# Performance work log

Measured on AMD Instinct MI355X. Metric: run time of the kernel, lower is better.

Reference implementation:

```python
import jax, jax.numpy as jnp
import numpy as np

B, L, DIM = 4, 4096, 1024
H, DQK, DV, DINNER, CHUNK = 16, 64, 64, 64, 64
BASE_LR, BASE_WD = 1e-3, 0.9


def setup_inputs() -> dict:
    key = jax.random.key(0)
    ks = jax.random.split(key, 9)
    def s(k, shape, scale):
        return jax.random.normal(k, shape, jnp.float32) * scale
    return {
        "x": jax.random.normal(ks[0], (B, L, DIM), jnp.float32),
        "Wq": s(ks[1], (H * DQK, DIM), DIM ** -0.5),
        "Wk": s(ks[2], (H * DQK, DIM), DIM ** -0.5),
        "Wv": s(ks[3], (H * DV, DIM), DIM ** -0.5),
        "Wlr": s(ks[4], (2 * H, DIM), DIM ** -0.5),
        "Wbeta": s(ks[5], (2 * H, DIM), DIM ** -0.5),
        "Wo": s(ks[6], (DIM, H * DV), (H * DV) ** -0.5),
        "W_in_init": s(ks[7], (1, DINNER, H, DQK), DQK ** -0.5),
        "W_out_init": s(ks[8], (1, DINNER, H, DV), DINNER ** -0.5),
    }


def reference(x, Wq, Wk, Wv, Wlr, Wbeta, Wo, W_in_init, W_out_init):
    b, l, _ = x.shape
    nc = l // CHUNK
    # projections + silu feature map on q/k (feature_map='silu')
    q = jax.nn.silu(x @ Wq.T).reshape(b, l, H, DQK)
    k = jax.nn.silu(x @ Wk.T).reshape(b, l, H, DQK)
    v = (x @ Wv.T).reshape(b, l, H, DV)
    # per-token, per-head gates: lr for (W_in, W_out) and weight-decay gates
    lr = jax.nn.sigmoid(x @ Wlr.T) * BASE_LR     # [b, l, 2H]
    wd = jax.nn.sigmoid(x @ Wbeta.T) * BASE_WD   # [b, l, 2H]

    def chunked(t):  # [b, l, ...] -> [nc, b, CHUNK, ...]
        return jnp.moveaxis(t.reshape(b, nc, CHUNK, *t.shape[2:]), 1, 0)

    qc, kc, vc = chunked(q), chunked(k), chunked(v)
    lr_c = chunked(lr).mean(axis=2)  # [nc, b, 2H], chunk-mean gate
    wd_c = chunked(wd).mean(axis=2)
    lr_in, lr_out = lr_c[..., :H], lr_c[..., H:]
    wd_in, wd_out = wd_c[..., :H], wd_c[..., H:]

    W_in0 = jnp.broadcast_to(W_in_init, (b, DINNER, H, DQK))
    W_out0 = jnp.broadcast_to(W_out_init, (b, DINNER, H, DV))

    def step(carry, xs):
        W_in, W_out = carry
        qi, ki, vi, li, lo, wi, wo = xs
        # readout with current fast weights (softmax over chunk dim n)
        p_q = jax.nn.softmax(jnp.einsum('bnhd,bDhd->bnhD', qi, W_in), axis=1)
        o = jnp.einsum('bnhD,bDhd->bnhd', p_q, W_out)
        # mlp_backprop(k, v, W_in, W_out): fast-weight gradients
        p = jax.nn.softmax(jnp.einsum('bnhd,bDhd->bnhD', ki, W_in), axis=1)
        grad_out = jnp.einsum('bnhD,bnhd->bDhd', -p, vi)
        a = jnp.einsum('bDhd,bnhd->bnhD', W_out, vi)
        s = jnp.sum(p * a, axis=-1, keepdims=True)
        g_z = -(p * a - p * s)
        grad_in = jnp.einsum('bnhd,bnhD->bDhd', ki, g_z)
        # decayed SGD update with data-dependent per-head gates
        W_in = wi[:, None, :, None] * W_in - li[:, None, :, None] * grad_in
        W_out = wo[:, None, :, None] * W_out - lo[:, None, :, None] * grad_out
        return (W_in, W_out), o

    _, outs = jax.lax.scan(step, (W_in0, W_out0),
                           (qc, kc, vc, lr_in, lr_out, wd_in, wd_out))
    # [nc, b, CHUNK, H, DV] -> [b, l, H*DV]
    o = jnp.moveaxis(outs, 0, 1).reshape(b, l, H * DV)
    return o @ Wo.T
```

## Files before the change

### kernel.cpp

```cpp
#include <hip/hip_runtime.h>
#include <stdint.h>

typedef unsigned short u16;
typedef uint32_t u32;
typedef __attribute__((ext_vector_type(4))) float f32x4;
typedef __attribute__((ext_vector_type(8))) short bf16x8;

#define DEVINL __device__ __forceinline__

DEVINL u16 f2bf(float f) {
    union { float f; u32 u; } a; a.f = f;
    u32 u = a.u;
    return (u16)((u + 0x7fffu + ((u >> 16) & 1u)) >> 16);
}
DEVINL u32 pk2(float a, float b) { return (u32)f2bf(a) | ((u32)f2bf(b) << 16); }

DEVINL u32 swz128(u32 row, u32 colb) { return row * 128u + (colb ^ ((row & 7u) << 4)); }

DEVINL void gload_lds16(const u16* g, char* l) {
    __builtin_amdgcn_global_load_lds(
        (const __attribute__((address_space(1))) void*)g,
        (__attribute__((address_space(3))) void*)l, 16, 0, 0);
}

DEVINL float frcp(float x) { float r; asm("v_rcp_f32 %0, %1" : "=v"(r) : "v"(x)); return r; }

template<int C> DEVINL float fdpp(float x) {
    union { float f; int i; } a, b; a.f = x;
    b.i = __builtin_amdgcn_update_dpp(0, a.i, C, 0xf, 0xf, false);
    return b.f;
}
DEVINL float rmax16(float v) {
    v = fmaxf(v, fdpp<0x128>(v)); v = fmaxf(v, fdpp<0x124>(v));
    v = fmaxf(v, fdpp<0x122>(v)); v = fmaxf(v, fdpp<0x121>(v)); return v;
}
DEVINL float rsum16(float v) {
    v += fdpp<0x128>(v); v += fdpp<0x124>(v);
    v += fdpp<0x122>(v); v += fdpp<0x121>(v); return v;
}

DEVINL f32x4 trans4(f32x4 v, int q) {
    float s0 = fdpp<0xB1>(v[0]), s1 = fdpp<0xB1>(v[1]),
          s2 = fdpp<0xB1>(v[2]), s3 = fdpp<0xB1>(v[3]);
    f32x4 t;
    bool q1 = (q & 1) != 0;
    t[0] = q1 ? s1 : v[0];
    t[1] = q1 ? v[1] : s0;
    t[2] = q1 ? s3 : v[2];
    t[3] = q1 ? v[3] : s2;
    float u0 = fdpp<0x4E>(t[0]), u1 = fdpp<0x4E>(t[1]),
          u2 = fdpp<0x4E>(t[2]), u3 = fdpp<0x4E>(t[3]);
    f32x4 r;
    bool q2 = (q & 2) != 0;
    r[0] = q2 ? u2 : t[0];
    r[1] = q2 ? u3 : t[1];
    r[2] = q2 ? t[2] : u0;
    r[3] = q2 ? t[3] : u1;
    return r;
}

__global__ __launch_bounds__(256) void convert_kernel(
    const float* __restrict__ x, const float* __restrict__ Wq,
    const float* __restrict__ Wk, const float* __restrict__ Wv,
    const float* __restrict__ Wo, const float* __restrict__ Wlr,
    const float* __restrict__ Wbeta,
    u16* __restrict__ xb, u16* __restrict__ wb, u16* __restrict__ wob,
    u16* __restrict__ wlb)
{
    const int t0 = blockIdx.x * 256 + threadIdx.x;
    const int stride = gridDim.x * 256;
    auto cv = [&](const float* src, u16* dst, int n4) {
        for (int i = t0; i < n4; i += stride) {
            float4 v = ((const float4*)src)[i];
            uint2 p;
            p.x = pk2(v.x, v.y);
            p.y = pk2(v.z, v.w);
            ((uint2*)dst)[i] = p;
        }
    };
    cv(x, xb, 4194304);
    cv(Wq, wb, 262144);
    cv(Wk, wb + 1048576, 262144);
    cv(Wv, wb + 2097152, 262144);
    cv(Wo, wob, 262144);
    cv(Wlr, wlb, 8192);
    cv(Wbeta, wlb + 32768, 8192);
}

__global__ __launch_bounds__(256) void proj_qkv_kernel(
    const u16* __restrict__ xb, const u16* __restrict__ wb,
    u16* __restrict__ qb, u16* __restrict__ kb, u16* __restrict__ vb)
{
    __shared__ __align__(16) char As[128 * 128];
    __shared__ __align__(16) char Bs[128 * 128];
    const int bn = blockIdx.x;
    const int bm = blockIdx.y;
    const int wsel = bn >> 3;
    u16* __restrict__ dst = (wsel == 0) ? qb : ((wsel == 1) ? kb : vb);
    const int cb = (bn & 7) * 128;
    const int wrow = bn * 128;
    const int rb = bm * 128;
    const int tid = threadIdx.x;
    const int lane = tid & 63;
    const int wv = tid >> 6;
    const int wr = (wv >> 1) * 64, wc = (wv & 1) * 64;
    const int li = lane & 15, g = lane >> 4;
    const int lr8 = lane >> 3, lc8 = lane & 7;

    f32x4 acc[4][4];
#pragma unroll
    for (int i = 0; i < 4; ++i)
#pragma unroll
        for (int j = 0; j < 4; ++j) acc[i][j] = (f32x4)0.0f;

    for (int k0 = 0; k0 < 1024; k0 += 64) {
        __syncthreads();
#pragma unroll
        for (int ld = 0; ld < 4; ++ld) {
            int r0 = wv * 32 + ld * 8;
            int rowT = r0 + lr8;
            int csw = (lc8 * 8) ^ ((rowT & 7) << 3);
            gload_lds16(xb + (size_t)(rb + rowT) * 1024 + k0 + csw, As + r0 * 128);
            gload_lds16(wb + (size_t)(wrow + rowT) * 1024 + k0 + csw, Bs + r0 * 128);
        }
        __syncthreads();
#pragma unroll
        for (int ks = 0; ks < 2; ++ks) {
            bf16x8 af[4], bfr[4];
#pragma unroll
            for (int m = 0; m < 4; ++m)
                af[m] = *(const bf16x8*)(As + swz128(wr + m * 16 + li, ks * 64 + g * 16));
#pragma unroll
            for (int n = 0; n < 4; ++n)
                bfr[n] = *(const bf16x8*)(Bs + swz128(wc + n * 16 + li, ks * 64 + g * 16));
#pragma unroll
            for (int m = 0; m < 4; ++m)
#pragma unroll
                for (int n = 0; n < 4; ++n)
                    acc[m][n] = __builtin_amdgcn_mfma_f32_16x16x32_bf16(af[m], bfr[n], acc[m][n], 0, 0, 0);
        }
    }
    const bool do_silu = (wsel < 2);
#pragma unroll
    for (int m = 0; m < 4; ++m) {
        int t = rb + wr + m * 16 + g * 4;
#pragma unroll
        for (int r = 0; r < 4; ++r) {
#pragma unroll
            for (int n = 0; n < 4; ++n) {
                float v = acc[m][n][r];
                if (do_silu) v = v / (1.0f + __expf(-v));
                int col = cb + wc + n * 16 + li;
                dst[(size_t)(t + r) * 1024 + col] = f2bf(v);
            }
        }
    }
}

__global__ __launch_bounds__(256) void lrwd_kernel(
    const u16* __restrict__ xb, const u16* __restrict__ wlb,
    float* __restrict__ lrc_all)
{
    __shared__ __align__(16) char As[128 * 128];
    __shared__ __align__(16) char Bs[64 * 128];
    __shared__ float red[128][65];
    const int bm = blockIdx.x;
    const int rb = bm * 128;
    const int tid = threadIdx.x;
    const int lane = tid & 63;
    const int wv = tid >> 6;
    const int li = lane & 15, g = lane >> 4;
    const int lr8 = lane >> 3, lc8 = lane & 7;

    f32x4 acc[2][4];
#pragma unroll
    for (int i = 0; i < 2; ++i)
#pragma unroll
        for (int j = 0; j < 4; ++j) acc[i][j] = (f32x4)0.0f;

    for (int k0 = 0; k0 < 1024; k0 += 64) {
        __syncthreads();
#pragma unroll
        for (int ld = 0; ld < 4; ++ld) {
            int r0 = wv * 32 + ld * 8;
            int rowT = r0 + lr8;
            int csw = (lc8 * 8) ^ ((rowT & 7) << 3);
            gload_lds16(xb + (size_t)(rb + rowT) * 1024 + k0 + csw, As + r0 * 128);
        }
#pragma unroll
        for (int ld = 0; ld < 2; ++ld) {
            int r0 = wv * 16 + ld * 8;
            int rowT = r0 + lr8;
            int csw = (lc8 * 8) ^ ((rowT & 7) << 3);
            gload_lds16(wlb + (size_t)rowT * 1024 + k0 + csw, Bs + r0 * 128);
        }
        __syncthreads();
#pragma unroll
        for (int ks = 0; ks < 2; ++ks) {
            bf16x8 af[2], bfr[4];
#pragma unroll
            for (int m = 0; m < 2; ++m)
                af[m] = *(const bf16x8*)(As + swz128(wv * 32 + m * 16 + li, ks * 64 + g * 16));
#pragma unroll
            for (int n = 0; n < 4; ++n)
                bfr[n] = *(const bf16x8*)(Bs + swz128(n * 16 + li, ks * 64 + g * 16));
#pragma unroll
            for (int m = 0; m < 2; ++m)
#pragma unroll
                for (int n = 0; n < 4; ++n)
                    acc[m][n] = __builtin_amdgcn_mfma_f32_16x16x32_bf16(af[m], bfr[n], acc[m][n], 0, 0, 0);
        }
    }
#pragma unroll
    for (int m = 0; m < 2; ++m) {
#pragma unroll
        for (int n = 0; n < 4; ++n) {
            int col = n * 16 + li;
            float scale = (col < 32) ? 1e-3f : 0.9f;
#pragma unroll
            for (int r = 0; r < 4; ++r) {
                int t = wv * 32 + m * 16 + g * 4 + r;
                float s = acc[m][n][r];
                red[t][col] = scale / (1.0f + __expf(-s));
            }
        }
    }
    __syncthreads();
    if (tid < 128) {
        int chunk = tid >> 6, col = tid & 63;
        float s = 0.f;
#pragma unroll
        for (int i = 0; i < 64; ++i) s += red[chunk * 64 + i][col];
        int b = bm >> 5;
        int cidx = (bm & 31) * 2 + chunk;
        lrc_all[((size_t)(b * 64 + cidx)) * 64 + col] = s * (1.0f / 64.0f);
    }
}

__global__ __launch_bounds__(512) void scan_kernel(
    const u16* __restrict__ qb, const u16* __restrict__ kb, const u16* __restrict__ vb,
    const float* __restrict__ lrc_all, const float* __restrict__ Wi0,
    const float* __restrict__ Wo0, u16* __restrict__ ob)
{
    const int bh = blockIdx.x;
    const int b = bh >> 4, h = bh & 15;
    const int tid = threadIdx.x;
    const int lane = tid & 63;
    const int w8 = tid >> 6;
    const bool isA = (w8 < 4);
    const int wq = w8;
    const int wk = w8 - 4;
    const int li = lane & 15, g = lane >> 4;
    const int q4 = li & 3, b4 = li & 12;

    __shared__ __align__(16) char SQ2[2][8192];
    __shared__ __align__(16) char Kc2[2][8192];
    __shared__ __align__(16) char Vc2[2][8192];
    __shared__ __align__(16) char KcT2[2][8192];
    __shared__ __align__(16) char VcT2[2][8192];
    __shared__ __align__(16) char SWoT2[2][8192];
    __shared__ __align__(16) char SWiN[8192];
    __shared__ __align__(16) char SWoN[8192];
    __shared__ __align__(16) char SPQ[8192];
    __shared__ __align__(16) char SPTN[8192];
    __shared__ __align__(16) char SGZN[8192];
    __shared__ float spart[256];
    __shared__ float lrc[256];
    __shared__ u32 cntA, cntB;

    if (tid == 0) { cntA = 0u; cntB = 0u; }

    f32x4 WiR[4], WoR[4];
    if (!isA) {
#pragma unroll
        for (int tn = 0; tn < 4; ++tn) {
            int d = tn * 16 + li;
#pragma unroll
            for (int r = 0; r < 4; ++r) {
                int D = wk * 16 + g * 4 + r;
                WiR[tn][r] = Wi0[((size_t)D * 16 + h) * 64 + d];
                WoR[tn][r] = Wo0[((size_t)D * 16 + h) * 64 + d];
            }
            *(uint2*)(SWoT2[0] + swz128(d, wk * 32 + g * 8)) =
                make_uint2(pk2(WoR[tn][0], WoR[tn][1]), pk2(WoR[tn][2], WoR[tn][3]));
            f32x4 ti = trans4(WiR[tn], q4);
            *(uint2*)(SWiN + swz128(wk * 16 + g * 4 + q4, tn * 32 + b4 * 2)) =
                make_uint2(pk2(ti[0], ti[1]), pk2(ti[2], ti[3]));
            f32x4 to = trans4(WoR[tn], q4);
            *(uint2*)(SWoN + swz128(wk * 16 + g * 4 + q4, tn * 32 + b4 * 2)) =
                make_uint2(pk2(to[0], to[1]), pk2(to[2], to[3]));
        }
    }
    if (tid < 256) {
        int cc = tid >> 2, j = tid & 3;
        lrc[cc * 4 + j] = lrc_all[((size_t)(b * 64 + cc)) * 64 + j * 16 + h];
    }

    const int nb4 = ((tid & 255) >> 4) * 4;
    const int db4 = (tid & 15) * 4;
    uint4 pq_[2];
    uint2 pk_[4], pv_[4];
    auto prefetch = [&](int c) {
        const size_t base = ((size_t)(b * 4096 + c * 64)) * 1024 + h * 64;
#pragma unroll
        for (int p = 0; p < 2; ++p) {
            int id = p * 256 + (tid & 255);
            int n = id >> 3;
            int d0 = (id & 7) * 8;
            pq_[p] = *(const uint4*)(qb + base + (size_t)n * 1024 + d0);
        }
#pragma unroll
        for (int j = 0; j < 4; ++j) {
            pk_[j] = *(const uint2*)(kb + base + (size_t)(nb4 + j) * 1024 + db4);
            pv_[j] = *(const uint2*)(vb + base + (size_t)(nb4 + j) * 1024 + db4);
        }
    };
    auto commit = [&](int buf) {
#pragma unroll
        for (int p = 0; p < 2; ++p) {
            int id = p * 256 + (tid & 255);
            int n = id >> 3;
            int d0 = (id & 7) * 8;
            *(uint4*)(SQ2[buf] + swz128(n, d0 * 2)) = pq_[p];
        }
#pragma unroll
        for (int j = 0; j < 4; ++j) {
            *(uint2*)(Kc2[buf] + swz128(nb4 + j, db4 * 2)) = pk_[j];
            *(uint2*)(Vc2[buf] + swz128(nb4 + j, db4 * 2)) = pv_[j];
        }
#pragma unroll
        for (int i = 0; i < 4; ++i) {
            u32 k0 = (((i & 2) ? pk_[0].y : pk_[0].x) >> ((i & 1) * 16)) & 0xffffu;
            u32 k1 = (((i & 2) ? pk_[1].y : pk_[1].x) >> ((i & 1) * 16)) & 0xffffu;
            u32 k2 = (((i & 2) ? pk_[2].y : pk_[2].x) >> ((i & 1) * 16)) & 0xffffu;
            u32 k3 = (((i & 2) ? pk_[3].y : pk_[3].x) >> ((i & 1) * 16)) & 0xffffu;
            *(uint2*)(KcT2[buf] + swz128(db4 + i, nb4 * 2)) =
                make_uint2(k0 | (k1 << 16), k2 | (k3 << 16));
            u32 v0 = (((i & 2) ? pv_[0].y : pv_[0].x) >> ((i & 1) * 16)) & 0xffffu;
            u32 v1 = (((i & 2) ? pv_[1].y : pv_[1].x) >> ((i & 1) * 16)) & 0xffffu;
            u32 v2 = (((i & 2) ? pv_[2].y : pv_[2].x) >> ((i & 1) * 16)) & 0xffffu;
            u32 v3 = (((i & 2) ? pv_[3].y : pv_[3].x) >> ((i & 1) * 16)) & 0xffffu;
            *(uint2*)(VcT2[buf] + swz128(db4 + i, nb4 * 2)) =
                make_uint2(v0 | (v1 << 16), v2 | (v3 << 16));
        }
    };

    if (isA) { prefetch(0); commit(0); }
    __syncthreads();

    for (int c = 0; c < 64; ++c) {
        const int cur = c & 1, nxt = cur ^ 1;
        f32x4 pk[4], aT[4], go[4];

        if (isA) {
            if (c + 1 < 64) prefetch(c + 1);
            bf16x8 wiA0 = *(const bf16x8*)(SWiN + swz128(wq * 16 + li, g * 16));
            bf16x8 wiA1 = *(const bf16x8*)(SWiN + swz128(wq * 16 + li, 64 + g * 16));
            f32x4 sq[4];
            __builtin_amdgcn_s_setprio(1);
#pragma unroll
            for (int tn = 0; tn < 4; ++tn) {
                bf16x8 b0 = *(const bf16x8*)(SQ2[cur] + swz128(tn * 16 + li, g * 16));
                bf16x8 b1 = *(const bf16x8*)(SQ2[cur] + swz128(tn * 16 + li, 64 + g * 16));
                f32x4 z = (f32x4)0.0f;
                z = __builtin_amdgcn_mfma_f32_16x16x32_bf16(wiA0, b0, z, 0, 0, 0);
                z = __builtin_amdgcn_mfma_f32_16x16x32_bf16(wiA1, b1, z, 0, 0, 0);
                sq[tn] = z;
            }
            __builtin_amdgcn_s_setprio(0);
#pragma unroll
            for (int r = 0; r < 4; ++r) {
                float m = fmaxf(fmaxf(sq[0][r], sq[1][r]), fmaxf(sq[2][r], sq[3][r]));
                m = rmax16(m);
                float e0 = __expf(sq[0][r] - m), e1 = __expf(sq[1][r] - m);
                float e2 = __expf(sq[2][r] - m), e3 = __expf(sq[3][r] - m);
                float inv = frcp(rsum16(e0 + e1 + e2 + e3));
                sq[0][r] = e0 * inv; sq[1][r] = e1 * inv; sq[2][r] = e2 * inv; sq[3][r] = e3 * inv;
            }
#pragma unroll
            for (int tn = 0; tn < 4; ++tn) {
                int n = tn * 16 + li;
                *(uint2*)(SPQ + swz128(n, (wq * 16 + g * 4) * 2)) =
                    make_uint2(pk2(sq[tn][0], sq[tn][1]), pk2(sq[tn][2], sq[tn][3]));
            }
            if (c + 1 < 64) commit(nxt);
            bf16x8 wob0[4], wob1[4];
#pragma unroll
            for (int tn = 0; tn < 4; ++tn) {
                wob0[tn] = *(const bf16x8*)(SWoT2[cur] + swz128(tn * 16 + li, g * 16));
                wob1[tn] = *(const bf16x8*)(SWoT2[cur] + swz128(tn * 16 + li, 64 + g * 16));
            }
            __threadfence_block();
            if (lane == 0) atomicAdd(&cntA, 1u);
            {
                volatile u32* vc = &cntA;
                u32 tgt = 4u * (u32)(c + 1);
                while (*vc < tgt) { __builtin_amdgcn_s_sleep(1); }
            }
            __threadfence_block();
            bf16x8 a0 = *(const bf16x8*)(SPQ + swz128(wq * 16 + li, g * 16));
            bf16x8 a1 = *(const bf16x8*)(SPQ + swz128(wq * 16 + li, 64 + g * 16));
            f32x4 o4[4];
            __builtin_amdgcn_s_setprio(1);
#pragma unroll
            for (int tn = 0; tn < 4; ++tn) {
                f32x4 z = (f32x4)0.0f;
                z = __builtin_amdgcn_mfma_f32_16x16x32_bf16(a0, wob0[tn], z, 0, 0, 0);
                z = __builtin_amdgcn_mfma_f32_16x16x32_bf16(a1, wob1[tn], z, 0, 0, 0);
                o4[tn] = z;
            }
            __builtin_amdgcn_s_setprio(0);
            const size_t obase = ((size_t)(b * 4096 + c * 64)) * 1024 + h * 64;
            const int n_ = wq * 16 + g * 4 + q4;
#pragma unroll
            for (int tn = 0; tn < 4; ++tn) {
                f32x4 to = trans4(o4[tn], q4);
                *(uint2*)(ob + obase + (size_t)n_ * 1024 + tn * 16 + b4) =
                    make_uint2(pk2(to[0], to[1]), pk2(to[2], to[3]));
            }
        } else {
            bf16x8 wiA0 = *(const bf16x8*)(SWiN + swz128(wk * 16 + li, g * 16));
            bf16x8 wiA1 = *(const bf16x8*)(SWiN + swz128(wk * 16 + li, 64 + g * 16));
            __builtin_amdgcn_s_setprio(1);
#pragma unroll
            for (int tn = 0; tn < 4; ++tn) {
                bf16x8 b0 = *(const bf16x8*)(Kc2[cur] + swz128(tn * 16 + li, g * 16));
                bf16x8 b1 = *(const bf16x8*)(Kc2[cur] + swz128(tn * 16 + li, 64 + g * 16));
                f32x4 z = (f32x4)0.0f;
                z = __builtin_amdgcn_mfma_f32_16x16x32_bf16(wiA0, b0, z, 0, 0, 0);
                z = __builtin_amdgcn_mfma_f32_16x16x32_bf16(wiA1, b1, z, 0, 0, 0);
                pk[tn] = z;
            }
            __builtin_amdgcn_s_setprio(0);
#pragma unroll
            for (int r = 0; r < 4; ++r) {
                float m = fmaxf(fmaxf(pk[0][r], pk[1][r]), fmaxf(pk[2][r], pk[3][r]));
                m = rmax16(m);
                float e0 = __expf(pk[0][r] - m), e1 = __expf(pk[1][r] - m);
                float e2 = __expf(pk[2][r] - m), e3 = __expf(pk[3][r] - m);
                float inv = frcp(rsum16(e0 + e1 + e2 + e3));
                pk[0][r] = e0 * inv; pk[1][r] = e1 * inv; pk[2][r] = e2 * inv; pk[3][r] = e3 * inv;
            }
            bf16x8 woA0 = *(const bf16x8*)(SWoN + swz128(wk * 16 + li, g * 16));
            bf16x8 woA1 = *(const bf16x8*)(SWoN + swz128(wk * 16 + li, 64 + g * 16));
            __builtin_amdgcn_s_setprio(1);
#pragma unroll
            for (int tn = 0; tn < 4; ++tn) {
                bf16x8 b0 = *(const bf16x8*)(Vc2[cur] + swz128(tn * 16 + li, g * 16));
                bf16x8 b1 = *(const bf16x8*)(Vc2[cur] + swz128(tn * 16 + li, 64 + g * 16));
                f32x4 z = (f32x4)0.0f;
                z = __builtin_amdgcn_mfma_f32_16x16x32_bf16(woA0, b0, z, 0, 0, 0);
                z = __builtin_amdgcn_mfma_f32_16x16x32_bf16(woA1, b1, z, 0, 0, 0);
                aT[tn] = z;
            }
            __builtin_amdgcn_s_setprio(0);
#pragma unroll
            for (int tn = 0; tn < 4; ++tn) {
                f32x4 t4 = pk[tn] * aT[tn];
                float s_ = t4[0] + t4[1] + t4[2] + t4[3];
                s_ += __shfl_xor(s_, 16);
                s_ += __shfl_xor(s_, 32);
                if (g == 0) spart[wk * 64 + tn * 16 + li] = s_;
            }
#pragma unroll
            for (int tn = 0; tn < 4; ++tn) {
                f32x4 tp = trans4(pk[tn], q4);
                *(uint2*)(SPTN + swz128(wk * 16 + g * 4 + q4, tn * 32 + b4 * 2)) =
                    make_uint2(pk2(tp[0], tp[1]), pk2(tp[2], tp[3]));
            }
            {
                bf16x8 a0 = *(const bf16x8*)(SPTN + swz128(wk * 16 + li, g * 16));
                bf16x8 a1 = *(const bf16x8*)(SPTN + swz128(wk * 16 + li, 64 + g * 16));
                __builtin_amdgcn_s_setprio(1);
#pragma unroll
                for (int tn = 0; tn < 4; ++tn) {
                    bf16x8 b0 = *(const bf16x8*)(VcT2[cur] + swz128(tn * 16 + li, g * 16));
                    bf16x8 b1 = *(const bf16x8*)(VcT2[cur] + swz128(tn * 16 + li, 64 + g * 16));
                    f32x4 z = (f32x4)0.0f;
                    z = __builtin_amdgcn_mfma_f32_16x16x32_bf16(a0, b0, z, 0, 0, 0);
                    z = __builtin_amdgcn_mfma_f32_16x16x32_bf16(a1, b1, z, 0, 0, 0);
                    go[tn] = z;
                }
                __builtin_amdgcn_s_setprio(0);
            }
            bf16x8 kb0[4], kb1[4];
#pragma unroll
            for (int tn = 0; tn < 4; ++tn) {
                kb0[tn] = *(const bf16x8*)(KcT2[cur] + swz128(tn * 16 + li, g * 16));
                kb1[tn] = *(const bf16x8*)(KcT2[cur] + swz128(tn * 16 + li, 64 + g * 16));
            }
            __threadfence_block();
            if (lane == 0) atomicAdd(&cntB, 1u);
            {
                volatile u32* vc = &cntB;
                u32 tgt = 4u * (u32)(c + 1);
                while (*vc < tgt) { __builtin_amdgcn_s_sleep(1); }
            }
            __threadfence_block();
            f32x4 gz[4];
#pragma unroll
            for (int tn = 0; tn < 4; ++tn) {
                int n = tn * 16 + li;
                float sn = spart[n] + spart[64 + n] + spart[128 + n] + spart[192 + n];
#pragma unroll
                for (int r = 0; r < 4; ++r) gz[tn][r] = pk[tn][r] * (sn - aT[tn][r]);
                f32x4 tg = trans4(gz[tn], q4);
                *(uint2*)(SGZN + swz128(wk * 16 + g * 4 + q4, tn * 32 + b4 * 2)) =
                    make_uint2(pk2(tg[0], tg[1]), pk2(tg[2], tg[3]));
            }
            f32x4 gi[4];
            {
                bf16x8 a0 = *(const bf16x8*)(SGZN + swz128(wk * 16 + li, g * 16));
                bf16x8 a1 = *(const bf16x8*)(SGZN + swz128(wk * 16 + li, 64 + g * 16));
                __builtin_amdgcn_s_setprio(1);
#pragma unroll
                for (int tn = 0; tn < 4; ++tn) {
                    f32x4 z = (f32x4)0.0f;
                    z = __builtin_amdgcn_mfma_f32_16x16x32_bf16(a0, kb0[tn], z, 0, 0, 0);
                    z = __builtin_amdgcn_mfma_f32_16x16x32_bf16(a1, kb1[tn], z, 0, 0, 0);
                    gi[tn] = z;
                }
                __builtin_amdgcn_s_setprio(0);
            }
            if (c + 1 < 64) {
                float lin = lrc[c * 4 + 0], lout = lrc[c * 4 + 1];
                float win = lrc[c * 4 + 2], wout = lrc[c * 4 + 3];
#pragma unroll
                for (int tn = 0; tn < 4; ++tn) {
                    WiR[tn] = win * WiR[tn] - lin * gi[tn];
                    WoR[tn] = wout * WoR[tn] + lout * go[tn];
                    int d = tn * 16 + li;
                    *(uint2*)(SWoT2[nxt] + swz128(d, wk * 32 + g * 8)) =
                        make_uint2(pk2(WoR[tn][0], WoR[tn][1]), pk2(WoR[tn][2], WoR[tn][3]));
                    f32x4 ti = trans4(WiR[tn], q4);
                    *(uint2*)(SWiN + swz128(wk * 16 + g * 4 + q4, tn * 32 + b4 * 2)) =
                        make_uint2(pk2(ti[0], ti[1]), pk2(ti[2], ti[3]));
                    f32x4 to = trans4(WoR[tn], q4);
                    *(uint2*)(SWoN + swz128(wk * 16 + g * 4 + q4, tn * 32 + b4 * 2)) =
                        make_uint2(pk2(to[0], to[1]), pk2(to[2], to[3]));
                }
            }
        }
        __syncthreads();
    }
}

__global__ __launch_bounds__(256) void out_proj_kernel(
    const u16* __restrict__ ob, const u16* __restrict__ wob, float* __restrict__ out)
{
    __shared__ __align__(16) char As[128 * 128];
    __shared__ __align__(16) char Bs[128 * 128];
    const int bn = blockIdx.x;
    const int bm = blockIdx.y;
    const int cb = bn * 128;
    const int rb = bm * 128;
    const int tid = threadIdx.x;
    const int lane = tid & 63;
    const int wv = tid >> 6;
    const int wr = (wv >> 1) * 64, wc = (wv & 1) * 64;
    const int li = lane & 15, g = lane >> 4;
    const int lr8 = lane >> 3, lc8 = lane & 7;

    f32x4 acc[4][4];
#pragma unroll
    for (int i = 0; i < 4; ++i)
#pragma unroll
        for (int j = 0; j < 4; ++j) acc[i][j] = (f32x4)0.0f;

    for (int k0 = 0; k0 < 1024; k0 += 64) {
        __syncthreads();
#pragma unroll
        for (int ld = 0; ld < 4; ++ld) {
            int r0 = wv * 32 + ld * 8;
            int rowT = r0 + lr8;
            int csw = (lc8 * 8) ^ ((rowT & 7) << 3);
            gload_lds16(ob + (size_t)(rb + rowT) * 1024 + k0 + csw, As + r0 * 128);
            gload_lds16(wob + (size_t)(cb + rowT) * 1024 + k0 + csw, Bs + r0 * 128);
        }
        __syncthreads();
#pragma unroll
        for (int ks = 0; ks < 2; ++ks) {
            bf16x8 af[4], bfr[4];
#pragma unroll
            for (int m = 0; m < 4; ++m)
                af[m] = *(const bf16x8*)(As + swz128(wr + m * 16 + li, ks * 64 + g * 16));
#pragma unroll
            for (int n = 0; n < 4; ++n)
                bfr[n] = *(const bf16x8*)(Bs + swz128(wc + n * 16 + li, ks * 64 + g * 16));
#pragma unroll
            for (int m = 0; m < 4; ++m)
#pragma unroll
                for (int n = 0; n < 4; ++n)
                    acc[m][n] = __builtin_amdgcn_mfma_f32_16x16x32_bf16(af[m], bfr[n], acc[m][n], 0, 0, 0);
        }
    }
#pragma unroll
    for (int m = 0; m < 4; ++m) {
        int t = rb + wr + m * 16 + g * 4;
#pragma unroll
        for (int r = 0; r < 4; ++r) {
#pragma unroll
            for (int n = 0; n < 4; ++n) {
                int col = cb + wc + n * 16 + li;
                out[(size_t)(t + r) * 1024 + col] = acc[m][n][r];
            }
        }
    }
}

extern "C" void kernel_launch(void* const* d_in, const int* in_sizes, int n_in,
                              void* d_out, int out_size, void* d_ws, size_t ws_size,
                              hipStream_t stream)
{
    const float* x     = (const float*)d_in[0];
    const float* Wq    = (const float*)d_in[1];
    const float* Wk    = (const float*)d_in[2];
    const float* Wv    = (const float*)d_in[3];
    const float* Wlr   = (const float*)d_in[4];
    const float* Wbeta = (const float*)d_in[5];
    const float* Wo    = (const float*)d_in[6];
    const float* Wi0   = (const float*)d_in[7];
    const float* Wo0   = (const float*)d_in[8];
    float* out = (float*)d_out;

    char* od = (char*)d_out;
    u16* xb  = (u16*)(od);
    u16* wb  = (u16*)(od + 33554432u);
    u16* wlb = (u16*)(od + 39845888u);

    char* ws = (char*)d_ws;
    u16* qb        = (u16*)(ws);
    u16* kb        = (u16*)(ws + 33554432u);
    u16* vb        = (u16*)(ws + 67108864u);
    u16* obuf      = (u16*)(ws + 100663296u);
    float* lrc_all = (float*)(ws + 134217728u);
    u16* wob       = (u16*)(ws + 134283264u);
    if (ws_size < 136380416u) return;

    convert_kernel<<<2048, 256, 0, stream>>>(x, Wq, Wk, Wv, Wo, Wlr, Wbeta,
                                             xb, wb, wob, wlb);
    proj_qkv_kernel<<<dim3(24, 128), 256, 0, stream>>>(xb, wb, qb, kb, vb);
    lrwd_kernel<<<128, 256, 0, stream>>>(xb, wlb, lrc_all);
    scan_kernel<<<64, 512, 0, stream>>>(qb, kb, vb, lrc_all, Wi0, Wo0, obuf);
    out_proj_kernel<<<dim3(8, 128), 256, 0, stream>>>(obuf, wob, out);
}
```

Before: 504.0 us.

## Rewrite QKV projection GEMM as 256x256 double-buffered pipelined tile with vectorized stores

The QKV projection GEMM moves from 128x128 tiles with 4 waves and a load-sync-compute loop to 256x256 tiles with 8 waves and double-buffered LDS. Global-to-LDS loads for k-tile kt+2 are interleaved with the MFMA phases through explicit waitcnt, sched_barrier and setprio calls. The epilogue transposes each accumulator fragment with the DPP-based trans4 helper so it can write packed 8-byte stores instead of scalar bf16 stores. The aim is to hide memory latency and raise MFMA utilisation. The cost is 128KB of LDS and more registers per block, and the grid shrinks to 768 blocks.

```diff
diff --git a/kernel.cpp b/kernel.cpp
--- a/kernel.cpp
+++ b/kernel.cpp
@@ -59,6 +59,14 @@
     return r;
 }
 
+#define LGW()  do { asm volatile("s_waitcnt lgkmcnt(0)" ::: "memory"); \
+                    __builtin_amdgcn_sched_barrier(0); } while (0)
+#define VMW(N) do { asm volatile("s_waitcnt vmcnt(" #N ")" ::: "memory"); \
+                    __builtin_amdgcn_sched_barrier(0); } while (0)
+#define BARRAW() do { __builtin_amdgcn_sched_barrier(0); \
+                      __builtin_amdgcn_s_barrier(); \
+                      __builtin_amdgcn_sched_barrier(0); } while (0)
+
 __global__ __launch_bounds__(256) void convert_kernel(
     const float* __restrict__ x, const float* __restrict__ Wq,
     const float* __restrict__ Wk, const float* __restrict__ Wv,
@@ -87,72 +95,124 @@
     cv(Wbeta, wlb + 32768, 8192);
 }
 
-__global__ __launch_bounds__(256) void proj_qkv_kernel(
+#define RDA(BUF, Q, AF)                                                       \
+    _Pragma("unroll")                                                         \
+    for (int i_ = 0; i_ < 2; ++i_)                                            \
+        _Pragma("unroll")                                                     \
+        for (int kk_ = 0; kk_ < 2; ++kk_)                                     \
+            AF[i_ * 2 + kk_] = *(const bf16x8*)(&A2[BUF][swz128(              \
+                wm * 128 + (2 * (Q) + i_) * 16 + li, kk_ * 64 + g * 16)]);
+
+#define PROJ_MFMA(Q, AF)                                                      \
+    __builtin_amdgcn_s_setprio(1);                                            \
+    _Pragma("unroll")                                                         \
+    for (int i_ = 0; i_ < 2; ++i_)                                            \
+        _Pragma("unroll")                                                     \
+        for (int nf_ = 0; nf_ < 4; ++nf_) {                                   \
+            acc[2 * (Q) + i_][nf_] = __builtin_amdgcn_mfma_f32_16x16x32_bf16( \
+                AF[i_ * 2 + 0], Bfr[nf_ * 2 + 0], acc[2 * (Q) + i_][nf_], 0, 0, 0); \
+            acc[2 * (Q) + i_][nf_] = __builtin_amdgcn_mfma_f32_16x16x32_bf16( \
+                AF[i_ * 2 + 1], Bfr[nf_ * 2 + 1], acc[2 * (Q) + i_][nf_], 0, 0, 0); \
+        }                                                                     \
+    __builtin_amdgcn_s_setprio(0);
+
+__global__ __launch_bounds__(512) void proj_qkv_kernel(
     const u16* __restrict__ xb, const u16* __restrict__ wb,
     u16* __restrict__ qb, u16* __restrict__ kb, u16* __restrict__ vb)
 {
-    __shared__ __align__(16) char As[128 * 128];
-    __shared__ __align__(16) char Bs[128 * 128];
+    __shared__ __align__(16) char A2[2][32768];
+    __shared__ __align__(16) char B2[2][32768];
     const int bn = blockIdx.x;
     const int bm = blockIdx.y;
-    const int wsel = bn >> 3;
+    const int wsel = bn >> 2;
     u16* __restrict__ dst = (wsel == 0) ? qb : ((wsel == 1) ? kb : vb);
-    const int cb = (bn & 7) * 128;
-    const int wrow = bn * 128;
-    const int rb = bm * 128;
+    const int cb = (bn & 3) * 256;
+    const int wrow = bn * 256;
+    const int rb = bm * 256;
     const int tid = threadIdx.x;
     const int lane = tid & 63;
-    const int wv = tid >> 6;
-    const int wr = (wv >> 1) * 64, wc = (wv & 1) * 64;
+    const int w8 = tid >> 6;
+    const int wm = w8 >> 2;
+    const int wn = w8 & 3;
     const int li = lane & 15, g = lane >> 4;
-    const int lr8 = lane >> 3, lc8 = lane & 7;
-
-    f32x4 acc[4][4];
-#pragma unroll
-    for (int i = 0; i < 4; ++i)
+    const int q4 = li & 3, b4 = li & 12;
+
+    const int srow = tid >> 3;
+    const int scol8 = (tid & 7) * 8;
+    auto stA = [&](int kt2, int pass, int buf) {
+        int rowT = pass * 64 + srow;
+        int csw = scol8 ^ ((rowT & 7) << 3);
+        gload_lds16(xb + (size_t)(rb + rowT) * 1024 + kt2 * 64 + csw,
+                    &A2[buf][pass * 8192 + tid * 16]);
+    };
+    auto stB = [&](int kt2, int pass, int buf) {
+        int rowT = pass * 64 + srow;
+        int csw = scol8 ^ ((rowT & 7) << 3);
+        gload_lds16(wb + (size_t)(wrow + rowT) * 1024 + kt2 * 64 + csw,
+                    &B2[buf][pass * 8192 + tid * 16]);
+    };
+
+    f32x4 acc[8][4];
+#pragma unroll
+    for (int i = 0; i < 8; ++i)
 #pragma unroll
         for (int j = 0; j < 4; ++j) acc[i][j] = (f32x4)0.0f;
 
-    for (int k0 = 0; k0 < 1024; k0 += 64) {
-        __syncthreads();
-#pragma unroll
-        for (int ld = 0; ld < 4; ++ld) {
-            int r0 = wv * 32 + ld * 8;
-            int rowT = r0 + lr8;
-            int csw = (lc8 * 8) ^ ((rowT & 7) << 3);
-            gload_lds16(xb + (size_t)(rb + rowT) * 1024 + k0 + csw, As + r0 * 128);
-            gload_lds16(wb + (size_t)(wrow + rowT) * 1024 + k0 + csw, Bs + r0 * 128);
-        }
-        __syncthreads();
-#pragma unroll
-        for (int ks = 0; ks < 2; ++ks) {
-            bf16x8 af[4], bfr[4];
-#pragma unroll
-            for (int m = 0; m < 4; ++m)
-                af[m] = *(const bf16x8*)(As + swz128(wr + m * 16 + li, ks * 64 + g * 16));
-#pragma unroll
-            for (int n = 0; n < 4; ++n)
-                bfr[n] = *(const bf16x8*)(Bs + swz128(wc + n * 16 + li, ks * 64 + g * 16));
-#pragma unroll
-            for (int m = 0; m < 4; ++m)
-#pragma unroll
-                for (int n = 0; n < 4; ++n)
-                    acc[m][n] = __builtin_amdgcn_mfma_f32_16x16x32_bf16(af[m], bfr[n], acc[m][n], 0, 0, 0);
-        }
-    }
+#pragma unroll
+    for (int p = 0; p < 4; ++p) { stA(0, p, 0); stB(0, p, 0); }
+#pragma unroll
+    for (int p = 0; p < 4; ++p) { stA(1, p, 1); stB(1, p, 1); }
+    VMW(8);
+    BARRAW();
+
+    for (int kt = 0; kt < 16; ++kt) {
+        const int buf = kt & 1;
+        const bool st = (kt + 2 < 16);
+        bf16x8 Bfr[8];
+#pragma unroll
+        for (int nf = 0; nf < 4; ++nf)
+#pragma unroll
+            for (int kk = 0; kk < 2; ++kk)
+                Bfr[nf * 2 + kk] = *(const bf16x8*)(&B2[buf][swz128(
+                    wn * 64 + nf * 16 + li, kk * 64 + g * 16)]);
+        bf16x8 Af0[4], Af1[4];
+        RDA(buf, 0, Af0);
+        LGW();
+        BARRAW();
+        RDA(buf, 1, Af1);
+        if (st) stB(kt + 2, 0, buf);
+        PROJ_MFMA(0, Af0);
+        LGW();
+        RDA(buf, 2, Af0);
+        if (st) stB(kt + 2, 1, buf);
+        PROJ_MFMA(1, Af1);
+        LGW();
+        RDA(buf, 3, Af1);
+        if (st) { stB(kt + 2, 2, buf); stB(kt + 2, 3, buf); }
+        PROJ_MFMA(2, Af0);
+        LGW();
+        BARRAW();
+        if (st) { stA(kt + 2, 0, buf); stA(kt + 2, 1, buf);
+                  stA(kt + 2, 2, buf); stA(kt + 2, 3, buf); }
+        PROJ_MFMA(3, Af1);
+        if (kt < 14) { VMW(8); } else if (kt == 14) { VMW(0); }
+        BARRAW();
+    }
+
     const bool do_silu = (wsel < 2);
 #pragma unroll
-    for (int m = 0; m < 4; ++m) {
-        int t = rb + wr + m * 16 + g * 4;
-#pragma unroll
-        for (int r = 0; r < 4; ++r) {
-#pragma unroll
-            for (int n = 0; n < 4; ++n) {
-                float v = acc[m][n][r];
-                if (do_silu) v = v / (1.0f + __expf(-v));
-                int col = cb + wc + n * 16 + li;
-                dst[(size_t)(t + r) * 1024 + col] = f2bf(v);
-            }
+    for (int mf = 0; mf < 8; ++mf) {
+        const int n_ = rb + wm * 128 + mf * 16 + g * 4 + q4;
+#pragma unroll
+        for (int nf = 0; nf < 4; ++nf) {
+            f32x4 o = acc[mf][nf];
+            if (do_silu) {
+#pragma unroll
+                for (int r = 0; r < 4; ++r) o[r] = o[r] / (1.0f + __expf(-o[r]));
+            }
+            f32x4 to = trans4(o, q4);
+            *(uint2*)(dst + (size_t)n_ * 1024 + cb + wn * 64 + nf * 16 + b4) =
+                make_uint2(pk2(to[0], to[1]), pk2(to[2], to[3]));
         }
     }
 }
@@ -639,7 +699,7 @@
 
     convert_kernel<<<2048, 256, 0, stream>>>(x, Wq, Wk, Wv, Wo, Wlr, Wbeta,
                                              xb, wb, wob, wlb);
-    proj_qkv_kernel<<<dim3(24, 128), 256, 0, stream>>>(xb, wb, qb, kb, vb);
+    proj_qkv_kernel<<<dim3(12, 64), 512, 0, stream>>>(xb, wb, qb, kb, vb);
     lrwd_kernel<<<128, 256, 0, stream>>>(xb, wlb, lrc_all);
     scan_kernel<<<64, 512, 0, stream>>>(qb, kb, vb, lrc_all, Wi0, Wo0, obuf);
     out_proj_kernel<<<dim3(8, 128), 256, 0, stream>>>(obuf, wob, out);
```

Measured after the change: 488.5 us. 3.1% less time.
